# Performance work log

Measured on AMD Instinct MI355X. Metric: run time of the kernel, lower is better.

The kernel has to match this reference:

```python
import jax, jax.numpy as jnp
from jax import lax
import numpy as np

B, L, E, D, A, M, V, T = 64, 196, 2048, 512, 512, 512, 30000, 21


def setup_inputs() -> dict:
    key = jax.random.key(0)
    ks = jax.random.split(key, 22)
    s = 0.02
    encoder_out = jax.random.normal(ks[0], (B, L, E), jnp.float32)
    captions = jax.random.randint(ks[1], (B, T), 0, V, dtype=jnp.int32)
    lens = jax.random.randint(ks[2], (B,), 2, T + 1, dtype=jnp.int32)
    caption_lengths = jnp.sort(lens)[::-1]  # descending, as torch loop requires
    p = {
        'W_enc': jax.random.normal(ks[3], (E, A)) * s, 'b_enc': jnp.zeros((A,)),
        'W_dec': jax.random.normal(ks[4], (D, A)) * s, 'b_dec': jnp.zeros((A,)),
        'w_att': jax.random.normal(ks[5], (A, 1)) * s, 'b_att': jnp.zeros((1,)),
        'emb': jax.random.uniform(ks[6], (V, M), minval=-0.1, maxval=0.1),
        'W_ih': jax.random.normal(ks[7], (M + E, 4 * D)) * s, 'b_ih': jnp.zeros((4 * D,)),
        'W_hh': jax.random.normal(ks[8], (D, 4 * D)) * s, 'b_hh': jnp.zeros((4 * D,)),
        'W_h0': jax.random.normal(ks[9], (E, D)) * s, 'b_h0': jnp.zeros((D,)),
        'W_c0': jax.random.normal(ks[10], (E, D)) * s, 'b_c0': jnp.zeros((D,)),
        'W_beta': jax.random.normal(ks[11], (D, E)) * s, 'b_beta': jnp.zeros((E,)),
        'W_fc': jax.random.uniform(ks[12], (D, V), minval=-0.1, maxval=0.1), 'b_fc': jnp.zeros((V,)),
    }
    return {'encoder_out': encoder_out, 'captions': captions,
            'caption_lengths': caption_lengths, **p}


def reference(encoder_out, captions, caption_lengths,
              W_enc, b_enc, W_dec, b_dec, w_att, b_att, emb,
              W_ih, b_ih, W_hh, b_hh, W_h0, b_h0, W_c0, b_c0,
              W_beta, b_beta, W_fc, b_fc):
    max_len = captions.shape[1] - 1  # teacher forcing: predict y_1..y_T
    x_emb = emb[captions]            # [B,T,M]  (dropout = identity in eval)

    mean_enc = encoder_out.mean(axis=1)
    h0 = jnp.tanh(mean_enc @ W_h0 + b_h0)
    c0 = jnp.tanh(mean_enc @ W_c0 + b_c0)

    # enc projection is constant across timesteps -> hoist out of the loop
    e_proj = encoder_out @ W_enc + b_enc  # [B,L,A]

    # mask[b,t] = (caption_lengths[b]-1) > t  (valid only because lens sorted desc,
    # matching the torch batch_t truncation exactly)
    mask = (caption_lengths[:, None] - 1) > jnp.arange(max_len)[None, :]

    def step(carry, xs):
        h, c = carry
        emb_t, m = xs  # [B,M], [B]
        d = h @ W_dec + b_dec                                   # [B,A]
        energy = (jax.nn.relu(e_proj + d[:, None, :]) @ w_att)[..., 0] + b_att[0]  # [B,L]
        alpha = jax.nn.softmax(energy, axis=1)
        ctx = jnp.einsum('ble,bl->be', encoder_out, alpha)      # [B,E]
        gate = jax.nn.sigmoid(h @ W_beta + b_beta)
        x = jnp.concatenate([emb_t, gate * ctx], axis=1)        # [B,M+E]
        gates = x @ W_ih + b_ih + h @ W_hh + b_hh               # [B,4D]
        i, f, g, o = jnp.split(gates, 4, axis=1)
        c_new = jax.nn.sigmoid(f) * c + jax.nn.sigmoid(i) * jnp.tanh(g)
        h_new = jax.nn.sigmoid(o) * jnp.tanh(c_new)
        pred = h_new @ W_fc + b_fc                              # [B,V]
        mf = m[:, None].astype(pred.dtype)
        return (h_new, c_new), (pred * mf, alpha * mf)

    xs = (jnp.swapaxes(x_emb[:, :max_len, :], 0, 1), mask.T)    # time-major
    _, (preds, alphas) = lax.scan(step, (h0, c0), xs)
    predictions = jnp.swapaxes(preds, 0, 1)                     # [B,max_len,V]
    alphas = jnp.swapaxes(alphas, 0, 1)                         # [B,max_len,L]
    return predictions, alphas
```

## Files before the change

kernel.cpp:

```cpp
#include <hip/hip_runtime.h>
#include <math.h>

namespace {

constexpr int NB  = 64;
constexpr int NL  = 196;
constexpr int NE  = 2048;
constexpr int ND  = 512;
constexpr int NA  = 512;
constexpr int NM  = 512;
constexpr int NV  = 30000;
constexpr int NT  = 21;
constexpr int NML = 20;
constexpr int NG  = 4 * ND;
constexpr int KXG = NM + NE;
constexpr int KSPL = 8, KSL = KXG / KSPL;
constexpr int NALL = ND + NE + NG + NV;
constexpr int OFF_GATE = ND;
constexpr int OFF_HWHH = ND + NE;
constexpr int OFF_PRED = ND + NE + NG;

constexpr size_t WS_MEAN = 0;
constexpr size_t WS_H    = WS_MEAN + (size_t)NB * NE;
constexpr size_t WS_C    = WS_H    + (size_t)NB * ND;
constexpr size_t WS_D    = WS_C    + (size_t)NB * ND;
constexpr size_t WS_GATE = WS_D    + (size_t)NB * NA;
constexpr size_t WS_HWHH = WS_GATE + (size_t)NB * NE;
constexpr size_t WS_EN   = WS_HWHH + (size_t)NB * NG;
constexpr size_t WS_PP   = WS_EN   + (size_t)NB * NL;
constexpr size_t WS_SHB  = WS_PP   + (size_t)1048576;
constexpr size_t SH_HBF  = 0;
constexpr size_t SH_XEMB = SH_HBF  + (size_t)NB * ND;
constexpr size_t SH_GCTX = SH_XEMB + (size_t)NML * NB * NM;
constexpr size_t SH_EPROJ= SH_GCTX + (size_t)NB * NE;
constexpr size_t SH_WET  = SH_EPROJ+ (size_t)NB * NL * NA;
constexpr size_t SH_WIHX = SH_WET  + (size_t)NA * NE;
constexpr size_t SH_WALL = SH_WIHX + (size_t)NG * KXG;
constexpr size_t SH_ENCBF= SH_WALL + (size_t)NALL * ND;
constexpr size_t SH_END  = SH_ENCBF+ (size_t)NB * NL * NE;
constexpr size_t BYTES_ENC = WS_SHB * 4 + SH_END * 2;

typedef __attribute__((ext_vector_type(8))) short short8v;
typedef __attribute__((ext_vector_type(4))) float f32x4;

__device__ __forceinline__ float sigmoidf_(float x) { return 1.f / (1.f + expf(-x)); }
__device__ __forceinline__ short f2bf(float f) {
  unsigned u = __float_as_uint(f);
  return (short)((u + 0x7FFFu + ((u >> 16) & 1u)) >> 16);
}
__device__ __forceinline__ float bf2f(short s) {
  return __uint_as_float(((unsigned)(unsigned short)s) << 16);
}


template <int R>
__device__ __forceinline__ void stage_bf16(const short* __restrict__ src, int ldK,
                                           int rowClamp, short* lds, int tid) {
#pragma unroll
  for (int cidx = tid; cidx < R * 8; cidx += 256) {
    int row = cidx >> 3, kb = cidx & 7;
    int r = row < rowClamp ? row : rowClamp;
    int4 v = *(const int4*)(src + (size_t)r * ldK + kb * 8);
    *(int4*)(lds + row * 64 + ((kb ^ (row & 7)) << 3)) = v;
  }
}

template <int R>
__device__ __forceinline__ void stage_f32cvt(const float* __restrict__ src, int ldK,
                                             short* lds, int tid) {
#pragma unroll
  for (int cidx = tid; cidx < R * 8; cidx += 256) {
    int row = cidx >> 3, kb = cidx & 7;
    const float* p = src + (size_t)row * ldK + kb * 8;
    float4 x = *(const float4*)p;
    float4 y = *(const float4*)(p + 4);
    short8v s;
    s[0] = f2bf(x.x); s[1] = f2bf(x.y); s[2] = f2bf(x.z); s[3] = f2bf(x.w);
    s[4] = f2bf(y.x); s[5] = f2bf(y.y); s[6] = f2bf(y.z); s[7] = f2bf(y.w);
    *(short8v*)(lds + row * 64 + ((kb ^ (row & 7)) << 3)) = s;
  }
}

template <int FM, int FN>
__device__ __forceinline__ void mma_tiles(const short* ldsA, const short* ldsB,
                                          int wr, int wc, int lane, f32x4 acc[FM][FN]) {
  int l15 = lane & 15;
#pragma unroll
  for (int kk = 0; kk < 2; ++kk) {
    int kb0 = kk * 4 + (lane >> 4);
    short8v a[FM], b[FN];
#pragma unroll
    for (int m = 0; m < FM; ++m) {
      int row = wr * FM * 16 + m * 16 + l15;
      a[m] = *(const short8v*)(ldsA + row * 64 + ((kb0 ^ (row & 7)) << 3));
    }
#pragma unroll
    for (int n = 0; n < FN; ++n) {
      int row = wc * FN * 16 + n * 16 + l15;
      b[n] = *(const short8v*)(ldsB + row * 64 + ((kb0 ^ (row & 7)) << 3));
    }
#pragma unroll
    for (int m = 0; m < FM; ++m)
#pragma unroll
      for (int n = 0; n < FN; ++n)
        acc[m][n] = __builtin_amdgcn_mfma_f32_16x16x32_bf16(a[m], b[n], acc[m][n], 0, 0, 0);
  }
}


__global__ __launch_bounds__(256) void k_tcvt(const float* __restrict__ src, int Ks, int Ns,
                                              short* __restrict__ dst, int ldDst, int kOff) {
  __shared__ float tbuf[32][33];
  int n0 = blockIdx.x * 32, k0 = blockIdx.y * 32;
  int tx = threadIdx.x, ty = threadIdx.y;
#pragma unroll
  for (int i = 0; i < 32; i += 8) {
    int k = k0 + ty + i, n = n0 + tx;
    tbuf[ty + i][tx] = (k < Ks && n < Ns) ? src[(size_t)k * Ns + n] : 0.f;
  }
  __syncthreads();
#pragma unroll
  for (int i = 0; i < 32; i += 8) {
    int n = n0 + ty + i, k = k0 + tx;
    if (n < Ns && k < Ks) dst[(size_t)n * ldDst + kOff + k] = f2bf(tbuf[tx][ty + i]);
  }
}

template <bool BF>
__global__ __launch_bounds__(256) void k_prep(const float* __restrict__ enc,
                                              short* __restrict__ encbf,
                                              float* __restrict__ mean_enc) {
  int b = blockIdx.y;
  int e = blockIdx.x * 256 + threadIdx.x;
  const float* p = enc + (size_t)b * NL * NE + e;
  short* q = encbf + (size_t)b * NL * NE + e;
  float s = 0.f;
  for (int l = 0; l < NL; ++l) {
    float v = p[(size_t)l * NE];
    s += v;
    if (BF) q[(size_t)l * NE] = f2bf(v);
  }
  mean_enc[(size_t)b * NE + e] = s * (1.f / NL);
}

__global__ void k_xemb(const int* __restrict__ caps, const float* __restrict__ emb,
                       short* __restrict__ xemb) {
  int i = blockIdx.x * 256 + threadIdx.x;
  int m = i & (NM - 1), b = (i >> 9) & (NB - 1), t = i >> 15;
  xemb[i] = f2bf(emb[(size_t)caps[b * NT + t] * NM + m]);
}

__global__ void k_init0(const float* __restrict__ mean_enc, const float* __restrict__ W_h0,
                        const float* __restrict__ W_c0, float* __restrict__ PP) {
  int idx = blockIdx.x * 256 + threadIdx.x;
  int ks = blockIdx.y;
  int b = idx >> 10, jh = idx & 1023, half = jh >> 9, j = jh & 511;
  const float* W = half ? W_c0 : W_h0;
  const float* mp = mean_enc + (size_t)b * NE + ks * 128;
  const float* Wp = W + (size_t)(ks * 128) * ND + j;
  float acc = 0.f;
#pragma unroll 4
  for (int k = 0; k < 128; ++k) acc = fmaf(mp[k], Wp[(size_t)k * ND], acc);
  PP[(size_t)ks * 65536 + idx] = acc;
}

__global__ void k_init1(const float* __restrict__ PP, const float* __restrict__ b_h0,
                        const float* __restrict__ b_c0, float* __restrict__ h,
                        float* __restrict__ c, short* __restrict__ h_bf) {
  int idx = blockIdx.x * 256 + threadIdx.x;
  int b = idx >> 9, j = idx & 511;
  float ah = b_h0[j], ac = b_c0[j];
  for (int s = 0; s < 16; ++s) {
    const float* p = PP + (size_t)s * 65536 + b * 1024;
    ah += p[j]; ac += p[512 + j];
  }
  float hv = tanhf(ah), cv = tanhf(ac);
  h[idx] = hv; c[idx] = cv; h_bf[idx] = f2bf(hv);
}

template <bool BF>
__global__ __launch_bounds__(256) void k_eproj(const float* __restrict__ enc,
                                               const short* __restrict__ encbf,
                                               const short* __restrict__ We_t,
                                               const float* __restrict__ b_enc,
                                               short* __restrict__ e_proj) {
  constexpr int FM = 4, FN = 4;
  __shared__ short ldsA[128 * 64], ldsB[128 * 64];
  int bm = blockIdx.x * 128, bn = blockIdx.y * 128;
  int tid = threadIdx.x, lane = tid & 63, wave = tid >> 6, wr = wave >> 1, wc = wave & 1;
  f32x4 acc[FM][FN];
#pragma unroll
  for (int m = 0; m < FM; ++m)
#pragma unroll
    for (int n = 0; n < FN; ++n) acc[m][n] = (f32x4){0.f, 0.f, 0.f, 0.f};
  for (int k0 = 0; k0 < NE; k0 += 64) {
    __syncthreads();
    if (BF) stage_bf16<128>(encbf + (size_t)bm * NE + k0, NE, 127, ldsA, tid);
    else    stage_f32cvt<128>(enc + (size_t)bm * NE + k0, NE, ldsA, tid);
    stage_bf16<128>(We_t + (size_t)bn * NE + k0, NE, 127, ldsB, tid);
    __syncthreads();
    mma_tiles<FM, FN>(ldsA, ldsB, wr, wc, lane, acc);
  }
#pragma unroll
  for (int m = 0; m < FM; ++m)
#pragma unroll
    for (int n = 0; n < FN; ++n) {
      int col = bn + wc * FN * 16 + n * 16 + (lane & 15);
      float bias = b_enc[col];
#pragma unroll
      for (int r = 0; r < 4; ++r) {
        int row = bm + wr * FM * 16 + m * 16 + (lane >> 4) * 4 + r;
        e_proj[(size_t)row * NA + col] = f2bf(acc[m][n][r] + bias);
      }
    }
}

__global__ __launch_bounds__(256) void k_hgemm(const short* __restrict__ h_bf,
                                               const short* __restrict__ Wall_t,
                                               const float* __restrict__ b_dec,
                                               const float* __restrict__ b_beta,
                                               const float* __restrict__ b_fc,
                                               const int* __restrict__ clen,
                                               float* __restrict__ d_buf,
                                               float* __restrict__ gate,
                                               float* __restrict__ hWhh,
                                               float* __restrict__ preds, int t) {
  constexpr int FM = 2, FN = 2;
  __shared__ short ldsA[64 * 64], ldsB[64 * 64];
  int bn = blockIdx.x * 64;
  int tid = threadIdx.x, lane = tid & 63, wave = tid >> 6, wr = wave >> 1, wc = wave & 1;
  int rowClampB = NALL - 1 - bn; if (rowClampB > 63) rowClampB = 63;
  f32x4 acc[FM][FN];
#pragma unroll
  for (int m = 0; m < FM; ++m)
#pragma unroll
    for (int n = 0; n < FN; ++n) acc[m][n] = (f32x4){0.f, 0.f, 0.f, 0.f};
  for (int k0 = 0; k0 < ND; k0 += 64) {
    __syncthreads();
    stage_bf16<64>(h_bf + k0, ND, 63, ldsA, tid);
    stage_bf16<64>(Wall_t + (size_t)bn * ND + k0, ND, rowClampB, ldsB, tid);
    __syncthreads();
    mma_tiles<FM, FN>(ldsA, ldsB, wr, wc, lane, acc);
  }
#pragma unroll
  for (int m = 0; m < FM; ++m)
#pragma unroll
    for (int r = 0; r < 4; ++r) {
      int row = wr * FM * 16 + m * 16 + (lane >> 4) * 4 + r;
      float mf = ((clen[row] - 1) > t) ? 1.f : 0.f;
#pragma unroll
      for (int n = 0; n < FN; ++n) {
        int col = bn + wc * FN * 16 + n * 16 + (lane & 15);
        float a = acc[m][n][r];
        if (bn < OFF_GATE) {
          d_buf[(size_t)row * NA + col] = a + b_dec[col];
        } else if (bn < OFF_HWHH) {
          int e = col - OFF_GATE;
          gate[(size_t)row * NE + e] = sigmoidf_(a + b_beta[e]);
        } else if (bn < OFF_PRED) {
          hWhh[(size_t)row * NG + (col - OFF_HWHH)] = a;
        } else {
          int v = col - OFF_PRED;
          if (v < NV) preds[((size_t)row * NML + t) * NV + v] = mf * (a + b_fc[v]);
        }
      }
    }
}


__global__ __launch_bounds__(256) void k_energy(const short* __restrict__ e_proj,
                                                const float* __restrict__ d_buf,
                                                const float* __restrict__ w_att,
                                                const float* __restrict__ b_att,
                                                float* __restrict__ energy) {
  int tid = threadIdx.x, wave = tid >> 6, lane = tid & 63;
  int row = blockIdx.x * 4 + wave;
  int b = row / NL;
  short8v ev = *(const short8v*)(e_proj + (size_t)row * NA + lane * 8);
  const float* dp = d_buf + (size_t)b * NA + lane * 8;
  float4 d0 = *(const float4*)dp, d1 = *(const float4*)(dp + 4);
  const float* wp = w_att + lane * 8;
  float4 w0 = *(const float4*)wp, w1 = *(const float4*)(wp + 4);
  float dd[8] = {d0.x, d0.y, d0.z, d0.w, d1.x, d1.y, d1.z, d1.w};
  float ww[8] = {w0.x, w0.y, w0.z, w0.w, w1.x, w1.y, w1.z, w1.w};
  float acc = 0.f;
#pragma unroll
  for (int i = 0; i < 8; ++i) {
    float v = bf2f(ev[i]) + dd[i];
    acc = fmaf(fmaxf(v, 0.f), ww[i], acc);
  }
#pragma unroll
  for (int off = 32; off; off >>= 1) acc += __shfl_down(acc, off);
  if (lane == 0) energy[row] = acc + b_att[0];
}

template <bool BF>
__global__ __launch_bounds__(256) void k_ctx(const short* __restrict__ encbf,
                                             const float* __restrict__ encf,
                                             const float* __restrict__ energy,
                                             const float* __restrict__ gate,
                                             const int* __restrict__ clen,
                                             short* __restrict__ gctx,
                                             float* __restrict__ alphas_out, int t) {
  int b = blockIdx.y, e0 = blockIdx.x * 512, tid = threadIdx.x;
  __shared__ float al[NL];
  __shared__ float red[8];
  int wave = tid >> 6, lane = tid & 63;
  float v = (tid < NL) ? energy[b * NL + tid] : -INFINITY;
  float mx = v;
#pragma unroll
  for (int off = 32; off; off >>= 1) mx = fmaxf(mx, __shfl_down(mx, off));
  if (lane == 0) red[wave] = mx;
  __syncthreads();
  if (tid == 0) red[0] = fmaxf(fmaxf(red[0], red[1]), fmaxf(red[2], red[3]));
  __syncthreads();
  mx = red[0];
  float ex = (tid < NL) ? expf(v - mx) : 0.f;
  float sm = ex;
#pragma unroll
  for (int off = 32; off; off >>= 1) sm += __shfl_down(sm, off);
  if (lane == 0) red[4 + wave] = sm;
  __syncthreads();
  if (tid == 0) red[0] = 1.f / (red[4] + red[5] + red[6] + red[7]);
  __syncthreads();
  float alv = ex * red[0];
  if (tid < NL) {
    al[tid] = alv;
    if (blockIdx.x == 0) {
      float mf = ((clen[b] - 1) > t) ? 1.f : 0.f;
      alphas_out[((size_t)b * NML + t) * NL + tid] = alv * mf;
    }
  }
  __syncthreads();
  float cx0 = 0.f, cx1 = 0.f;
  if (BF) {
    const unsigned* p = (const unsigned*)(encbf + (size_t)b * NL * NE + e0) + tid;
#pragma unroll 4
    for (int l = 0; l < NL; ++l) {
      unsigned u = p[(size_t)l * (NE / 2)];
      cx0 = fmaf(al[l], bf2f((short)(u & 0xffffu)), cx0);
      cx1 = fmaf(al[l], bf2f((short)(u >> 16)), cx1);
    }
  } else {
    const float* p = encf + (size_t)b * NL * NE + e0 + 2 * tid;
#pragma unroll 4
    for (int l = 0; l < NL; ++l) {
      float2 u = *(const float2*)(p + (size_t)l * NE);
      cx0 = fmaf(al[l], u.x, cx0);
      cx1 = fmaf(al[l], u.y, cx1);
    }
  }
  int e = e0 + 2 * tid;
  const float* gp = gate + (size_t)b * NE + e;
  unsigned out = (unsigned)(unsigned short)f2bf(cx0 * gp[0]) |
                 ((unsigned)(unsigned short)f2bf(cx1 * gp[1]) << 16);
  *(unsigned*)(gctx + (size_t)b * NE + e) = out;
}

__global__ __launch_bounds__(256) void k_gates(const short* __restrict__ xemb_t,
                                               const short* __restrict__ gctx,
                                               const short* __restrict__ Wihx_t,
                                               float* __restrict__ P) {
  constexpr int FM = 2, FN = 2;
  __shared__ short ldsA[64 * 64], ldsB[64 * 64];
  int bn = blockIdx.x * 64, ks = blockIdx.y;
  int tid = threadIdx.x, lane = tid & 63, wave = tid >> 6, wr = wave >> 1, wc = wave & 1;
  f32x4 acc[FM][FN];
#pragma unroll
  for (int m = 0; m < FM; ++m)
#pragma unroll
    for (int n = 0; n < FN; ++n) acc[m][n] = (f32x4){0.f, 0.f, 0.f, 0.f};
  int kend = (ks + 1) * KSL;
  for (int k0 = ks * KSL; k0 < kend; k0 += 64) {
    __syncthreads();
    if (k0 < NM) stage_bf16<64>(xemb_t + k0, NM, 63, ldsA, tid);
    else         stage_bf16<64>(gctx + (k0 - NM), NE, 63, ldsA, tid);
    stage_bf16<64>(Wihx_t + (size_t)bn * KXG + k0, KXG, 63, ldsB, tid);
    __syncthreads();
    mma_tiles<FM, FN>(ldsA, ldsB, wr, wc, lane, acc);
  }
#pragma unroll
  for (int m = 0; m < FM; ++m)
#pragma unroll
    for (int n = 0; n < FN; ++n) {
      int col = bn + wc * FN * 16 + n * 16 + (lane & 15);
#pragma unroll
      for (int r = 0; r < 4; ++r) {
        int row = wr * FM * 16 + m * 16 + (lane >> 4) * 4 + r;
        P[((size_t)ks * NB + row) * NG + col] = acc[m][n][r];
      }
    }
}

__global__ void k_lstm(const float* __restrict__ P, const float* __restrict__ hWhh,
                       const float* __restrict__ b_ih, const float* __restrict__ b_hh,
                       float* __restrict__ h, float* __restrict__ c,
                       short* __restrict__ h_bf) {
  int idx = blockIdx.x * 256 + threadIdx.x;
  int b = idx >> 9, j = idx & (ND - 1);
  const float* hw = hWhh + (size_t)b * NG;
  float gi = b_ih[j] + b_hh[j] + hw[j];
  float gf = b_ih[j + ND] + b_hh[j + ND] + hw[j + ND];
  float gg = b_ih[j + 2 * ND] + b_hh[j + 2 * ND] + hw[j + 2 * ND];
  float go = b_ih[j + 3 * ND] + b_hh[j + 3 * ND] + hw[j + 3 * ND];
  for (int s = 0; s < KSPL; ++s) {
    const float* Pp = P + ((size_t)s * NB + b) * NG;
    gi += Pp[j]; gf += Pp[j + ND]; gg += Pp[j + 2 * ND]; go += Pp[j + 3 * ND];
  }
  float cn = sigmoidf_(gf) * c[idx] + sigmoidf_(gi) * tanhf(gg);
  float hn = sigmoidf_(go) * tanhf(cn);
  c[idx] = cn;
  h[idx] = hn;
  h_bf[idx] = f2bf(hn);
}

}

extern "C" void kernel_launch(void* const* d_in, const int* in_sizes, int n_in,
                              void* d_out, int out_size, void* d_ws, size_t ws_size,
                              hipStream_t stream) {
  (void)in_sizes; (void)n_in; (void)out_size;
  const float* enc    = (const float*)d_in[0];
  const int*   caps   = (const int*)d_in[1];
  const int*   clen   = (const int*)d_in[2];
  const float* W_enc  = (const float*)d_in[3];
  const float* b_enc  = (const float*)d_in[4];
  const float* W_dec  = (const float*)d_in[5];
  const float* b_dec  = (const float*)d_in[6];
  const float* w_att  = (const float*)d_in[7];
  const float* b_att  = (const float*)d_in[8];
  const float* emb    = (const float*)d_in[9];
  const float* W_ih   = (const float*)d_in[10];
  const float* b_ih   = (const float*)d_in[11];
  const float* W_hh   = (const float*)d_in[12];
  const float* b_hh   = (const float*)d_in[13];
  const float* W_h0   = (const float*)d_in[14];
  const float* b_h0   = (const float*)d_in[15];
  const float* W_c0   = (const float*)d_in[16];
  const float* b_c0   = (const float*)d_in[17];
  const float* W_beta = (const float*)d_in[18];
  const float* b_beta = (const float*)d_in[19];
  const float* W_fc   = (const float*)d_in[20];
  const float* b_fc   = (const float*)d_in[21];

  float* ws     = (float*)d_ws;
  float* preds  = (float*)d_out;
  float* alphas = preds + (size_t)NB * NML * NV;

  float* mean_enc = ws + WS_MEAN;
  float* h        = ws + WS_H;
  float* c        = ws + WS_C;
  float* d_buf    = ws + WS_D;
  float* gate     = ws + WS_GATE;
  float* hWhh     = ws + WS_HWHH;
  float* energy   = ws + WS_EN;
  float* PP       = ws + WS_PP;
  short* shb      = (short*)(ws + WS_SHB);
  short* h_bf     = shb + SH_HBF;
  short* xemb     = shb + SH_XEMB;
  short* gctx     = shb + SH_GCTX;
  short* e_proj   = shb + SH_EPROJ;
  short* We_t     = shb + SH_WET;
  short* Wihx_t   = shb + SH_WIHX;
  short* Wall_t   = shb + SH_WALL;
  short* encbf    = shb + SH_ENCBF;
  const bool use_bf = ws_size >= BYTES_ENC;

  k_tcvt<<<dim3(NA / 32, NE / 32), dim3(32, 8), 0, stream>>>(W_enc, NE, NA, We_t, NE, 0);
  k_tcvt<<<dim3(NG / 32, KXG / 32), dim3(32, 8), 0, stream>>>(W_ih, KXG, NG, Wihx_t, KXG, 0);
  k_tcvt<<<dim3(NA / 32, ND / 32), dim3(32, 8), 0, stream>>>(W_dec, ND, NA, Wall_t, ND, 0);
  k_tcvt<<<dim3(NE / 32, ND / 32), dim3(32, 8), 0, stream>>>(
      W_beta, ND, NE, Wall_t + (size_t)OFF_GATE * ND, ND, 0);
  k_tcvt<<<dim3(NG / 32, ND / 32), dim3(32, 8), 0, stream>>>(
      W_hh, ND, NG, Wall_t + (size_t)OFF_HWHH * ND, ND, 0);
  k_tcvt<<<dim3((NV + 31) / 32, ND / 32), dim3(32, 8), 0, stream>>>(
      W_fc, ND, NV, Wall_t + (size_t)OFF_PRED * ND, ND, 0);
  if (use_bf)
    k_prep<true><<<dim3(NE / 256, NB), 256, 0, stream>>>(enc, encbf, mean_enc);
  else
    k_prep<false><<<dim3(NE / 256, NB), 256, 0, stream>>>(enc, encbf, mean_enc);
  k_xemb<<<(NML * NB * NM) / 256, 256, 0, stream>>>(caps, emb, xemb);

  k_init0<<<dim3(256, 16), 256, 0, stream>>>(mean_enc, W_h0, W_c0, PP);
  k_init1<<<(NB * ND) / 256, 256, 0, stream>>>(PP, b_h0, b_c0, h, c, h_bf);
  if (use_bf)
    k_eproj<true><<<dim3((NB * NL) / 128, NA / 128), 256, 0, stream>>>(enc, encbf, We_t,
                                                                       b_enc, e_proj);
  else
    k_eproj<false><<<dim3((NB * NL) / 128, NA / 128), 256, 0, stream>>>(enc, encbf, We_t,
                                                                        b_enc, e_proj);
  k_hgemm<<<OFF_PRED / 64, 256, 0, stream>>>(h_bf, Wall_t, b_dec, b_beta, b_fc, clen,
                                             d_buf, gate, hWhh, preds, 0);

  for (int t = 0; t < NML; ++t) {
    k_energy<<<(NB * NL) / 4, 256, 0, stream>>>(e_proj, d_buf, w_att, b_att, energy);
    if (use_bf)
      k_ctx<true><<<dim3(NE / 512, NB), 256, 0, stream>>>(encbf, enc, energy, gate, clen,
                                                          gctx, alphas, t);
    else
      k_ctx<false><<<dim3(NE / 512, NB), 256, 0, stream>>>(encbf, enc, energy, gate, clen,
                                                           gctx, alphas, t);
    k_gates<<<dim3(NG / 64, KSPL), 256, 0, stream>>>(xemb + (size_t)t * NB * NM, gctx,
                                                     Wihx_t, PP);
    k_lstm<<<(NB * ND) / 256, 256, 0, stream>>>(PP, hWhh, b_ih, b_hh, h, c, h_bf);
    k_hgemm<<<(NALL + 63) / 64, 256, 0, stream>>>(h_bf, Wall_t, b_dec, b_beta, b_fc, clen,
                                                  d_buf, gate, hWhh, preds, t);
  }
}
```

Before: 1.347 ms.

## Fold h@W_hh into gates GEMM, fuse LSTM cell via last-block reduction

Result: slower. 1.746 ms (+29.6%).

```diff
diff --git a/kernel.cpp b/kernel.cpp
--- a/kernel.cpp
+++ b/kernel.cpp
@@ -13,24 +13,24 @@
 constexpr int NT  = 21;
 constexpr int NML = 20;
 constexpr int NG  = 4 * ND;
-constexpr int KXG = NM + NE;
+constexpr int KXG = NM + NE + ND;
 constexpr int KSPL = 8, KSL = KXG / KSPL;
-constexpr int NALL = ND + NE + NG + NV;
+constexpr int NALL = ND + NE + NV;
 constexpr int OFF_GATE = ND;
-constexpr int OFF_HWHH = ND + NE;
-constexpr int OFF_PRED = ND + NE + NG;
+constexpr int OFF_PRED = ND + NE;
 
 constexpr size_t WS_MEAN = 0;
-constexpr size_t WS_H    = WS_MEAN + (size_t)NB * NE;
-constexpr size_t WS_C    = WS_H    + (size_t)NB * ND;
-constexpr size_t WS_D    = WS_C    + (size_t)NB * ND;
+constexpr size_t WS_C0   = WS_MEAN + (size_t)NB * NE;
+constexpr size_t WS_C1   = WS_C0   + (size_t)NB * ND;
+constexpr size_t WS_D    = WS_C1   + (size_t)NB * ND;
 constexpr size_t WS_GATE = WS_D    + (size_t)NB * NA;
-constexpr size_t WS_HWHH = WS_GATE + (size_t)NB * NE;
-constexpr size_t WS_EN   = WS_HWHH + (size_t)NB * NG;
-constexpr size_t WS_PP   = WS_EN   + (size_t)NB * NL;
+constexpr size_t WS_EN   = WS_GATE + (size_t)NB * NE;
+constexpr size_t WS_CNT  = WS_EN   + (size_t)NB * NL;
+constexpr size_t WS_PP   = WS_CNT  + 64;
 constexpr size_t WS_SHB  = WS_PP   + (size_t)1048576;
-constexpr size_t SH_HBF  = 0;
-constexpr size_t SH_XEMB = SH_HBF  + (size_t)NB * ND;
+constexpr size_t SH_HB0  = 0;
+constexpr size_t SH_HB1  = SH_HB0  + (size_t)NB * ND;
+constexpr size_t SH_XEMB = SH_HB1  + (size_t)NB * ND;
 constexpr size_t SH_GCTX = SH_XEMB + (size_t)NML * NB * NM;
 constexpr size_t SH_EPROJ= SH_GCTX + (size_t)NB * NE;
 constexpr size_t SH_WET  = SH_EPROJ+ (size_t)NB * NL * NA;
@@ -53,15 +53,23 @@
 }
 
 
+__device__ __forceinline__ void gload16(const short* g, short* l) {
+  __builtin_amdgcn_global_load_lds(
+      (const __attribute__((address_space(1))) unsigned int*)(g),
+      (__attribute__((address_space(3))) unsigned int*)(l), 16, 0, 0);
+}
+
 template <int R>
-__device__ __forceinline__ void stage_bf16(const short* __restrict__ src, int ldK,
-                                           int rowClamp, short* lds, int tid) {
-#pragma unroll
-  for (int cidx = tid; cidx < R * 8; cidx += 256) {
-    int row = cidx >> 3, kb = cidx & 7;
+__device__ __forceinline__ void stage_direct(const short* __restrict__ src, int ldK,
+                                             int rowClamp, short* lds, int tid) {
+  int wv = tid >> 6, lane = tid & 63;
+  int sub = lane >> 3;
+  int kb  = (lane & 7) ^ sub;
+#pragma unroll
+  for (int g = wv; g < R / 8; g += 4) {
+    int row = g * 8 + sub;
     int r = row < rowClamp ? row : rowClamp;
-    int4 v = *(const int4*)(src + (size_t)r * ldK + kb * 8);
-    *(int4*)(lds + row * 64 + ((kb ^ (row & 7)) << 3)) = v;
+    gload16(src + (size_t)r * ldK + (kb << 3), lds + g * 512);
   }
 }
 
@@ -108,6 +116,7 @@
 }
 
 
+template <bool PERM>
 __global__ __launch_bounds__(256) void k_tcvt(const float* __restrict__ src, int Ks, int Ns,
                                               short* __restrict__ dst, int ldDst, int kOff) {
   __shared__ float tbuf[32][33];
@@ -122,8 +131,15 @@
 #pragma unroll
   for (int i = 0; i < 32; i += 8) {
     int n = n0 + ty + i, k = k0 + tx;
-    if (n < Ns && k < Ks) dst[(size_t)n * ldDst + kOff + k] = f2bf(tbuf[tx][ty + i]);
-  }
+    if (n < Ns && k < Ks) {
+      int nd = PERM ? (((n & 511) << 2) | (n >> 9)) : n;
+      dst[(size_t)nd * ldDst + kOff + k] = f2bf(tbuf[tx][ty + i]);
+    }
+  }
+}
+
+__global__ void k_zero(int* __restrict__ cnt) {
+  if (threadIdx.x < 32) cnt[threadIdx.x] = 0;
 }
 
 template <bool BF>
@@ -165,8 +181,8 @@
 }
 
 __global__ void k_init1(const float* __restrict__ PP, const float* __restrict__ b_h0,
-                        const float* __restrict__ b_c0, float* __restrict__ h,
-                        float* __restrict__ c, short* __restrict__ h_bf) {
+                        const float* __restrict__ b_c0, float* __restrict__ c0,
+                        short* __restrict__ hb0) {
   int idx = blockIdx.x * 256 + threadIdx.x;
   int b = idx >> 9, j = idx & 511;
   float ah = b_h0[j], ac = b_c0[j];
@@ -174,8 +190,8 @@
     const float* p = PP + (size_t)s * 65536 + b * 1024;
     ah += p[j]; ac += p[512 + j];
   }
-  float hv = tanhf(ah), cv = tanhf(ac);
-  h[idx] = hv; c[idx] = cv; h_bf[idx] = f2bf(hv);
+  c0[idx] = tanhf(ac);
+  hb0[idx] = f2bf(tanhf(ah));
 }
 
 template <bool BF>
@@ -186,7 +202,9 @@
                                                short* __restrict__ e_proj) {
   constexpr int FM = 4, FN = 4;
   __shared__ short ldsA[128 * 64], ldsB[128 * 64];
-  int bm = blockIdx.x * 128, bn = blockIdx.y * 128;
+  int p = blockIdx.x;
+  int l = (p & 7) * 49 + (p >> 3);
+  int bn = (l & 3) * 128, bm = (l >> 2) * 128;
   int tid = threadIdx.x, lane = tid & 63, wave = tid >> 6, wr = wave >> 1, wc = wave & 1;
   f32x4 acc[FM][FN];
 #pragma unroll
@@ -195,9 +213,9 @@
     for (int n = 0; n < FN; ++n) acc[m][n] = (f32x4){0.f, 0.f, 0.f, 0.f};
   for (int k0 = 0; k0 < NE; k0 += 64) {
     __syncthreads();
-    if (BF) stage_bf16<128>(encbf + (size_t)bm * NE + k0, NE, 127, ldsA, tid);
+    if (BF) stage_direct<128>(encbf + (size_t)bm * NE + k0, NE, 127, ldsA, tid);
     else    stage_f32cvt<128>(enc + (size_t)bm * NE + k0, NE, ldsA, tid);
-    stage_bf16<128>(We_t + (size_t)bn * NE + k0, NE, 127, ldsB, tid);
+    stage_direct<128>(We_t + (size_t)bn * NE + k0, NE, 127, ldsB, tid);
     __syncthreads();
     mma_tiles<FM, FN>(ldsA, ldsB, wr, wc, lane, acc);
   }
@@ -222,8 +240,7 @@
                                                const float* __restrict__ b_fc,
                                                const int* __restrict__ clen,
                                                float* __restrict__ d_buf,
-                                               float* __restrict__ gate,
-                                               float* __restrict__ hWhh,
+                                               float* __restrict__ gatebuf,
                                                float* __restrict__ preds, int t) {
   constexpr int FM = 2, FN = 2;
   __shared__ short ldsA[64 * 64], ldsB[64 * 64];
@@ -237,8 +254,8 @@
     for (int n = 0; n < FN; ++n) acc[m][n] = (f32x4){0.f, 0.f, 0.f, 0.f};
   for (int k0 = 0; k0 < ND; k0 += 64) {
     __syncthreads();
-    stage_bf16<64>(h_bf + k0, ND, 63, ldsA, tid);
-    stage_bf16<64>(Wall_t + (size_t)bn * ND + k0, ND, rowClampB, ldsB, tid);
+    stage_direct<64>(h_bf + k0, ND, 63, ldsA, tid);
+    stage_direct<64>(Wall_t + (size_t)bn * ND + k0, ND, rowClampB, ldsB, tid);
     __syncthreads();
     mma_tiles<FM, FN>(ldsA, ldsB, wr, wc, lane, acc);
   }
@@ -254,11 +271,9 @@
         float a = acc[m][n][r];
         if (bn < OFF_GATE) {
           d_buf[(size_t)row * NA + col] = a + b_dec[col];
-        } else if (bn < OFF_HWHH) {
+        } else if (bn < OFF_PRED) {
           int e = col - OFF_GATE;
-          gate[(size_t)row * NE + e] = sigmoidf_(a + b_beta[e]);
-        } else if (bn < OFF_PRED) {
-          hWhh[(size_t)row * NG + (col - OFF_HWHH)] = a;
+          gatebuf[(size_t)row * NE + e] = sigmoidf_(a + b_beta[e]);
         } else {
           int v = col - OFF_PRED;
           if (v < NV) preds[((size_t)row * NML + t) * NV + v] = mf * (a + b_fc[v]);
@@ -298,7 +313,7 @@
 __global__ __launch_bounds__(256) void k_ctx(const short* __restrict__ encbf,
                                              const float* __restrict__ encf,
                                              const float* __restrict__ energy,
-                                             const float* __restrict__ gate,
+                                             const float* __restrict__ gatebuf,
                                              const int* __restrict__ clen,
                                              short* __restrict__ gctx,
                                              float* __restrict__ alphas_out, int t) {
@@ -351,7 +366,7 @@
     }
   }
   int e = e0 + 2 * tid;
-  const float* gp = gate + (size_t)b * NE + e;
+  const float* gp = gatebuf + (size_t)b * NE + e;
   unsigned out = (unsigned)(unsigned short)f2bf(cx0 * gp[0]) |
                  ((unsigned)(unsigned short)f2bf(cx1 * gp[1]) << 16);
   *(unsigned*)(gctx + (size_t)b * NE + e) = out;
@@ -359,11 +374,19 @@
 
 __global__ __launch_bounds__(256) void k_gates(const short* __restrict__ xemb_t,
                                                const short* __restrict__ gctx,
+                                               const short* __restrict__ h_prev,
                                                const short* __restrict__ Wihx_t,
-                                               float* __restrict__ P) {
+                                               float* __restrict__ P,
+                                               int* __restrict__ cnt,
+                                               const float* __restrict__ b_ih,
+                                               const float* __restrict__ b_hh,
+                                               const float* __restrict__ c_prev,
+                                               float* __restrict__ c_next,
+                                               short* __restrict__ h_next) {
   constexpr int FM = 2, FN = 2;
   __shared__ short ldsA[64 * 64], ldsB[64 * 64];
-  int bn = blockIdx.x * 64, ks = blockIdx.y;
+  __shared__ int isLast;
+  int bnb = blockIdx.x, bn = bnb * 64, ks = blockIdx.y;
   int tid = threadIdx.x, lane = tid & 63, wave = tid >> 6, wr = wave >> 1, wc = wave & 1;
   f32x4 acc[FM][FN];
 #pragma unroll
@@ -372,10 +395,13 @@
     for (int n = 0; n < FN; ++n) acc[m][n] = (f32x4){0.f, 0.f, 0.f, 0.f};
   int kend = (ks + 1) * KSL;
   for (int k0 = ks * KSL; k0 < kend; k0 += 64) {
+    const short* asrc; int aldk;
+    if (k0 < NM)           { asrc = xemb_t + k0;              aldk = NM; }
+    else if (k0 < NM + NE) { asrc = gctx + (k0 - NM);         aldk = NE; }
+    else                   { asrc = h_prev + (k0 - NM - NE);  aldk = ND; }
     __syncthreads();
-    if (k0 < NM) stage_bf16<64>(xemb_t + k0, NM, 63, ldsA, tid);
-    else         stage_bf16<64>(gctx + (k0 - NM), NE, 63, ldsA, tid);
-    stage_bf16<64>(Wihx_t + (size_t)bn * KXG + k0, KXG, 63, ldsB, tid);
+    stage_direct<64>(asrc, aldk, 63, ldsA, tid);
+    stage_direct<64>(Wihx_t + (size_t)bn * KXG + k0, KXG, 63, ldsB, tid);
     __syncthreads();
     mma_tiles<FM, FN>(ldsA, ldsB, wr, wc, lane, acc);
   }
@@ -390,28 +416,31 @@
         P[((size_t)ks * NB + row) * NG + col] = acc[m][n][r];
       }
     }
-}
-
-__global__ void k_lstm(const float* __restrict__ P, const float* __restrict__ hWhh,
-                       const float* __restrict__ b_ih, const float* __restrict__ b_hh,
-                       float* __restrict__ h, float* __restrict__ c,
-                       short* __restrict__ h_bf) {
-  int idx = blockIdx.x * 256 + threadIdx.x;
-  int b = idx >> 9, j = idx & (ND - 1);
-  const float* hw = hWhh + (size_t)b * NG;
-  float gi = b_ih[j] + b_hh[j] + hw[j];
-  float gf = b_ih[j + ND] + b_hh[j + ND] + hw[j + ND];
-  float gg = b_ih[j + 2 * ND] + b_hh[j + 2 * ND] + hw[j + 2 * ND];
-  float go = b_ih[j + 3 * ND] + b_hh[j + 3 * ND] + hw[j + 3 * ND];
-  for (int s = 0; s < KSPL; ++s) {
-    const float* Pp = P + ((size_t)s * NB + b) * NG;
-    gi += Pp[j]; gf += Pp[j + ND]; gg += Pp[j + 2 * ND]; go += Pp[j + 3 * ND];
-  }
-  float cn = sigmoidf_(gf) * c[idx] + sigmoidf_(gi) * tanhf(gg);
-  float hn = sigmoidf_(go) * tanhf(cn);
-  c[idx] = cn;
-  h[idx] = hn;
-  h_bf[idx] = f2bf(hn);
+  __threadfence();
+  __syncthreads();
+  if (tid == 0) isLast = (atomicAdd(&cnt[bnb], 1) == KSPL - 1);
+  __syncthreads();
+  if (!isLast) return;
+  __threadfence();
+  for (int pr = tid; pr < NB * 16; pr += 256) {
+    int b = pr >> 4, jj = pr & 15;
+    int j = bnb * 16 + jj;
+    float gi = 0.f, gf = 0.f, gg = 0.f, go = 0.f;
+#pragma unroll
+    for (int s = 0; s < KSPL; ++s) {
+      float4 v = *(const float4*)&P[((size_t)s * NB + b) * NG + bn + jj * 4];
+      gi += v.x; gf += v.y; gg += v.z; go += v.w;
+    }
+    gi += b_ih[j] + b_hh[j];
+    gf += b_ih[j + ND] + b_hh[j + ND];
+    gg += b_ih[j + 2 * ND] + b_hh[j + 2 * ND];
+    go += b_ih[j + 3 * ND] + b_hh[j + 3 * ND];
+    float cn = sigmoidf_(gf) * c_prev[b * ND + j] + sigmoidf_(gi) * tanhf(gg);
+    float hn = sigmoidf_(go) * tanhf(cn);
+    c_next[b * ND + j] = cn;
+    h_next[b * ND + j] = f2bf(hn);
+  }
+  if (tid == 0) cnt[bnb] = 0;
 }
 
 }
@@ -448,15 +477,14 @@
   float* alphas = preds + (size_t)NB * NML * NV;
 
   float* mean_enc = ws + WS_MEAN;
-  float* h        = ws + WS_H;
-  float* c        = ws + WS_C;
+  float* cbuf[2]  = {ws + WS_C0, ws + WS_C1};
   float* d_buf    = ws + WS_D;
-  float* gate     = ws + WS_GATE;
-  float* hWhh     = ws + WS_HWHH;
+  float* gatebuf  = ws + WS_GATE;
   float* energy   = ws + WS_EN;
+  int*   cnt      = (int*)(ws + WS_CNT);
   float* PP       = ws + WS_PP;
   short* shb      = (short*)(ws + WS_SHB);
-  short* h_bf     = shb + SH_HBF;
+  short* hbuf[2]  = {shb + SH_HB0, shb + SH_HB1};
   short* xemb     = shb + SH_XEMB;
   short* gctx     = shb + SH_GCTX;
   short* e_proj   = shb + SH_EPROJ;
@@ -466,15 +494,17 @@
   short* encbf    = shb + SH_ENCBF;
   const bool use_bf = ws_size >= BYTES_ENC;
 
-  k_tcvt<<<dim3(NA / 32, NE / 32), dim3(32, 8), 0, stream>>>(W_enc, NE, NA, We_t, NE, 0);
-  k_tcvt<<<dim3(NG / 32, KXG / 32), dim3(32, 8), 0, stream>>>(W_ih, KXG, NG, Wihx_t, KXG, 0);
-  k_tcvt<<<dim3(NA / 32, ND / 32), dim3(32, 8), 0, stream>>>(W_dec, ND, NA, Wall_t, ND, 0);
-  k_tcvt<<<dim3(NE / 32, ND / 32), dim3(32, 8), 0, stream>>>(
+  k_tcvt<false><<<dim3(NA / 32, NE / 32), dim3(32, 8), 0, stream>>>(W_enc, NE, NA, We_t, NE, 0);
+  k_tcvt<true><<<dim3(NG / 32, (NM + NE) / 32), dim3(32, 8), 0, stream>>>(
+      W_ih, NM + NE, NG, Wihx_t, KXG, 0);
+  k_tcvt<true><<<dim3(NG / 32, ND / 32), dim3(32, 8), 0, stream>>>(
+      W_hh, ND, NG, Wihx_t, KXG, NM + NE);
+  k_tcvt<false><<<dim3(NA / 32, ND / 32), dim3(32, 8), 0, stream>>>(W_dec, ND, NA, Wall_t, ND, 0);
+  k_tcvt<false><<<dim3(NE / 32, ND / 32), dim3(32, 8), 0, stream>>>(
       W_beta, ND, NE, Wall_t + (size_t)OFF_GATE * ND, ND, 0);
-  k_tcvt<<<dim3(NG / 32, ND / 32), dim3(32, 8), 0, stream>>>(
-      W_hh, ND, NG, Wall_t + (size_t)OFF_HWHH * ND, ND, 0);
-  k_tcvt<<<dim3((NV + 31) / 32, ND / 32), dim3(32, 8), 0, stream>>>(
+  k_tcvt<false><<<dim3((NV + 31) / 32, ND / 32), dim3(32, 8), 0, stream>>>(
       W_fc, ND, NV, Wall_t + (size_t)OFF_PRED * ND, ND, 0);
+  k_zero<<<1, 64, 0, stream>>>(cnt);
   if (use_bf)
     k_prep<true><<<dim3(NE / 256, NB), 256, 0, stream>>>(enc, encbf, mean_enc);
   else
@@ -482,28 +512,30 @@
   k_xemb<<<(NML * NB * NM) / 256, 256, 0, stream>>>(caps, emb, xemb);
 
   k_init0<<<dim3(256, 16), 256, 0, stream>>>(mean_enc, W_h0, W_c0, PP);
-  k_init1<<<(NB * ND) / 256, 256, 0, stream>>>(PP, b_h0, b_c0, h, c, h_bf);
+  k_init1<<<(NB * ND) / 256, 256, 0, stream>>>(PP, b_h0, b_c0, cbuf[0], hbuf[0]);
   if (use_bf)
-    k_eproj<true><<<dim3((NB * NL) / 128, NA / 128), 256, 0, stream>>>(enc, encbf, We_t,
-                                                                       b_enc, e_proj);
+    k_eproj<true><<<392, 256, 0, stream>>>(enc, encbf, We_t, b_enc, e_proj);
   else
-    k_eproj<false><<<dim3((NB * NL) / 128, NA / 128), 256, 0, stream>>>(enc, encbf, We_t,
-                                                                        b_enc, e_proj);
-  k_hgemm<<<OFF_PRED / 64, 256, 0, stream>>>(h_bf, Wall_t, b_dec, b_beta, b_fc, clen,
-                                             d_buf, gate, hWhh, preds, 0);
+    k_eproj<false><<<392, 256, 0, stream>>>(enc, encbf, We_t, b_enc, e_proj);
+  k_hgemm<<<OFF_PRED / 64, 256, 0, stream>>>(hbuf[0], Wall_t, b_dec, b_beta, b_fc, clen,
+                                             d_buf, gatebuf, preds, 0);
 
   for (int t = 0; t < NML; ++t) {
+    short* h_prev = hbuf[t & 1];
+    short* h_next = hbuf[1 - (t & 1)];
+    float* c_prev = cbuf[t & 1];
+    float* c_next = cbuf[1 - (t & 1)];
     k_energy<<<(NB * NL) / 4, 256, 0, stream>>>(e_proj, d_buf, w_att, b_att, energy);
     if (use_bf)
-      k_ctx<true><<<dim3(NE / 512, NB), 256, 0, stream>>>(encbf, enc, energy, gate, clen,
-                                                          gctx, alphas, t);
+      k_ctx<true><<<dim3(NE / 512, NB), 256, 0, stream>>>(encbf, enc, energy, gatebuf,
+                                                          clen, gctx, alphas, t);
     else
-      k_ctx<false><<<dim3(NE / 512, NB), 256, 0, stream>>>(encbf, enc, energy, gate, clen,
-                                                           gctx, alphas, t);
+      k_ctx<false><<<dim3(NE / 512, NB), 256, 0, stream>>>(encbf, enc, energy, gatebuf,
+                                                           clen, gctx, alphas, t);
     k_gates<<<dim3(NG / 64, KSPL), 256, 0, stream>>>(xemb + (size_t)t * NB * NM, gctx,
-                                                     Wihx_t, PP);
-    k_lstm<<<(NB * ND) / 256, 256, 0, stream>>>(PP, hWhh, b_ih, b_hh, h, c, h_bf);
-    k_hgemm<<<(NALL + 63) / 64, 256, 0, stream>>>(h_bf, Wall_t, b_dec, b_beta, b_fc, clen,
-                                                  d_buf, gate, hWhh, preds, t);
-  }
-}
+                                                     h_prev, Wihx_t, PP, cnt, b_ih, b_hh,
+                                                     c_prev, c_next, h_next);
+    k_hgemm<<<(NALL + 63) / 64, 256, 0, stream>>>(h_next, Wall_t, b_dec, b_beta, b_fc,
+                                                  clen, d_buf, gatebuf, preds, t);
+  }
+}
```
